# Kernel tuning notes

Measured on AMD Instinct MI355X. Metric: run time of the kernel, lower is better.

## Reference

```python
import jax, jax.numpy as jnp
import numpy as np


def setup_inputs() -> dict:
    key = jax.random.key(0)
    ks = jax.random.split(key, 5)
    B, D, W = 8, 768, 128
    scale = 1.0 / np.sqrt(D)
    return {
        "x": jax.random.normal(ks[0], (B, D, W, W), dtype=jnp.float32),
        "in_proj_w": jax.random.normal(ks[1], (3 * D, D), dtype=jnp.float32) * scale,
        "in_proj_b": jax.random.normal(ks[2], (3 * D,), dtype=jnp.float32) * 0.01,
        "out_w": jax.random.normal(ks[3], (D, D), dtype=jnp.float32) * scale,
        "out_b": jax.random.normal(ks[4], (D,), dtype=jnp.float32) * 0.01,
        "num_heads": 12,
        "num_tokens": 8,
    }


def reference(x, in_proj_w, in_proj_b, out_w, out_b, num_heads, num_tokens):
    B, D, Wd, Hd = x.shape
    nt = num_tokens
    gs = Hd // nt            # grid (block) size
    T = nt * nt              # number of blocks / queries
    S = gs * gs              # k/v tokens per block
    h = num_heads
    hd = D // h

    # ---- query: adaptive avg pool to (nt, nt), flatten, permute -> (B, T, D)
    q = x.reshape(B, D, nt, gs, nt, gs).mean(axis=(3, 5))      # (B, D, nt, nt)
    q = q.reshape(B, D, T).transpose(0, 2, 1)                   # (B, T, D)

    # ---- key/value: faithful reproduction of unfold + view(x.size()) + reshape
    # torch: kv_perm (B,W,H,D) -> unfold -> (B, nt, nt, D, gs, gs) contiguous,
    # then reinterpreted flat as (B, W*H, D) (scrambles channel/pixel layout).
    t = x.transpose(0, 2, 3, 1)                                 # (B, W, H, D)
    t = t.reshape(B, nt, gs, nt, gs, D).transpose(0, 1, 3, 5, 2, 4)  # (B,nt,nt,D,gs,gs)
    kv = t.reshape(B, T, S, D)                                  # chunked into T blocks of S tokens

    # ---- in-projections (torch MultiheadAttention packed weights)
    Wq, Wk, Wv = in_proj_w[:D], in_proj_w[D:2 * D], in_proj_w[2 * D:]
    bq, bk, bv = in_proj_b[:D], in_proj_b[D:2 * D], in_proj_b[2 * D:]
    qp = (q @ Wq.T + bq).reshape(B, T, h, hd)                   # (B, T, h, hd)
    kp = (kv @ Wk.T + bk).reshape(B, T, S, h, hd)               # (B, T, S, h, hd)
    vp = (kv @ Wv.T + bv).reshape(B, T, S, h, hd)

    # ---- block-local single-query attention, batched over all T blocks
    scores = jnp.einsum("bthd,btshd->bths", qp, kp) / np.sqrt(hd)  # (B, T, h, S)
    attn = jax.nn.softmax(scores, axis=-1)
    ctx = jnp.einsum("bths,btshd->bthd", attn, vp).reshape(B, T, D)

    # ---- out projection
    return ctx @ out_w.T + out_b                                # (B, T, D)
```

## Files before the change

kernel.cpp:

```cpp
#include <hip/hip_runtime.h>
#include <hip/hip_bf16.h>

#define D_ 768
#define W_ 128
#define T_ 64
#define S_ 256
#define H_ 12
#define HH_ 6
#define BT_ 512

__device__ __forceinline__ unsigned short f2bf(float f) {
  unsigned u = __float_as_uint(f);
  u = (u + 0x7FFFu + ((u >> 16) & 1u)) >> 16;
  return (unsigned short)u;
}
__device__ __forceinline__ float bfu(unsigned s) {
  return __uint_as_float(s << 16);
}

__global__ __launch_bounds__(384) void k_pack(const float* __restrict__ x,
                                              unsigned short* __restrict__ packed,
                                              float* __restrict__ q) {
  const int blk  = blockIdx.x;
  const int cc   = blk & 15;
  const int tjp  = (blk >> 4) & 3;
  const int ti   = (blk >> 6) & 7;
  const int b    = blk >> 9;
  const int tid  = threadIdx.x;
  const int c8   = tid & 7;
  const int ch   = tid >> 3;
  const int btl  = c8 >> 2;
  const int btg0 = b*64 + ti*8 + tjp*2;
  const int ch0  = cc * 48;

  __shared__ unsigned short tile[48][2][260];
  __shared__ float poolsc[48][2];

  const float* xcol = x + (size_t)b*D_*16384 + (size_t)(ch0 + ch)*16384
                        + (16*ti)*128 + 32*tjp + c8*4;

  float psum = 0.f;
  #pragma unroll
  for (int r = 0; r < 16; ++r) {
    const float4 v = *(const float4*)(xcol + r*128);
    const int px = r*16 + (c8 & 3)*4;
    unsigned lo = (unsigned)f2bf(v.x) | ((unsigned)f2bf(v.y) << 16);
    unsigned hi = (unsigned)f2bf(v.z) | ((unsigned)f2bf(v.w) << 16);
    *(uint2*)&tile[ch][btl][px] = make_uint2(lo, hi);
    psum += (v.x + v.y) + (v.z + v.w);
  }
  psum += __shfl_xor(psum, 1);
  psum += __shfl_xor(psum, 2);
  if ((c8 & 3) == 0) poolsc[ch][btl] = psum;
  __syncthreads();

  for (int ii = tid; ii < 512; ii += 384) {
    const int bl = ii >> 8, p = ii & 255;
    unsigned short* pbt = packed + ((size_t)(btg0 + bl)*16 + cc)*D_*16;
    #pragma unroll
    for (int c = 0; c < 3; ++c) {
      unsigned u[8];
      #pragma unroll
      for (int k2 = 0; k2 < 8; ++k2) {
        const unsigned a  = tile[3*(2*k2)     + c][bl][p];
        const unsigned b2 = tile[3*(2*k2 + 1) + c][bl][p];
        u[k2] = a | (b2 << 16);
      }
      unsigned short* dst = pbt + (size_t)(c*256 + p)*16;
      *(uint4*)(dst)     = make_uint4(u[0], u[1], u[2], u[3]);
      *(uint4*)(dst + 8) = make_uint4(u[4], u[5], u[6], u[7]);
    }
  }
  if (tid < 96) {
    const int ch2 = tid >> 1, bl = tid & 1;
    q[(size_t)(btg0 + bl)*D_ + ch0 + ch2] = poolsc[ch2][bl] * (1.0f/256.0f);
  }
}

__global__ __launch_bounds__(256) void k_qkf(const float* __restrict__ q,
                                             const float* __restrict__ ipw,
                                             const float* __restrict__ ipb,
                                             unsigned short* __restrict__ qkout) {
  const int h   = blockIdx.x >> 5;
  const int btc = blockIdx.x & 31;
  const int bt0 = btc * 16;
  const int tid = threadIdx.x;
  const int i = tid & 63, qw = tid >> 6;
  __shared__ float wt[64][65];
  __shared__ float at[16][65];
  __shared__ float qps[16][72];

  {
    const float* Wr = ipw + (size_t)h*64*D_;
    float acc[4] = {0,0,0,0};
    for (int dc = 0; dc < D_; dc += 64) {
      #pragma unroll
      for (int k = 0; k < 4; ++k) {
        const int idx = k*256 + tid;
        const int r = idx >> 4, c4 = idx & 15;
        *(float4*)&wt[r][c4*4] = *(const float4*)(Wr + (size_t)r*D_ + dc + c4*4);
      }
      {
        const int r = tid >> 4, c4 = tid & 15;
        *(float4*)&at[r][c4*4] = *(const float4*)(q + (size_t)(bt0 + r)*D_ + dc + c4*4);
      }
      __syncthreads();
      #pragma unroll
      for (int dd = 0; dd < 64; ++dd) {
        const float wv = wt[i][dd];
        #pragma unroll
        for (int k = 0; k < 4; ++k)
          acc[k] += at[qw + k*4][dd] * wv;
      }
      __syncthreads();
    }
    const float bqv = ipb[h*64 + i];
    #pragma unroll
    for (int k = 0; k < 4; ++k)
      qps[qw + k*4][i] = acc[k] + bqv;
  }
  __syncthreads();

  for (int ddc = 0; ddc < D_; ddc += 64) {
    #pragma unroll
    for (int k = 0; k < 4; ++k) {
      const int idx = k*256 + tid;
      const int r = idx >> 4, c4 = idx & 15;
      *(float4*)&wt[r][c4*4] = *(const float4*)(ipw + (size_t)(D_ + h*64 + r)*D_ + ddc + c4*4);
    }
    __syncthreads();
    float acc2[4] = {0,0,0,0};
    #pragma unroll 8
    for (int kk = 0; kk < 64; ++kk) {
      const float w = wt[kk][i];
      #pragma unroll
      for (int k = 0; k < 4; ++k)
        acc2[k] += qps[qw + k*4][kk] * w;
    }
    #pragma unroll
    for (int k = 0; k < 4; ++k)
      qkout[((size_t)(bt0 + qw + k*4)*H_ + h)*D_ + ddc + i] = f2bf(acc2[k] * 0.125f);
    __syncthreads();
  }
}

__global__ __launch_bounds__(256) void k_attn3(const unsigned short* __restrict__ packed,
                                               const unsigned short* __restrict__ qkin,
                                               float* __restrict__ wout) {
  const int bt = blockIdx.x >> 1;
  const int hg = blockIdx.x & 1;
  const int tid = threadIdx.x;
  const int wv = tid >> 6, lane = tid & 63;
  __shared__ float pool_lds[HH_ * D_];
  __shared__ float sc[HH_][S_];

  {
    const uint4* src = (const uint4*)(qkin + ((size_t)bt*H_ + hg*HH_)*D_);
    #pragma unroll
    for (int k = 0; k < 3; ++k) {
      const int idx = k*256 + tid;
      if (idx < 576) {
        const uint4 v = src[idx];
        float* d = pool_lds + idx*8;
        d[0] = bfu(v.x & 0xFFFFu); d[1] = bfu(v.x >> 16);
        d[2] = bfu(v.y & 0xFFFFu); d[3] = bfu(v.y >> 16);
        d[4] = bfu(v.z & 0xFFFFu); d[5] = bfu(v.z >> 16);
        d[6] = bfu(v.w & 0xFFFFu); d[7] = bfu(v.w >> 16);
      }
    }
  }
  __syncthreads();

  float acc[HH_][4];
  #pragma unroll
  for (int h = 0; h < HH_; ++h)
    #pragma unroll
    for (int j = 0; j < 4; ++j) acc[h][j] = 0.f;

  {
    const unsigned short* pb = packed + ((size_t)bt*16 + (lane >> 2))*D_*16 + (lane & 3)*4;
    const int d0 = wv * 192;
    short4 pv[4];
    #pragma unroll
    for (int dd = 0; dd < 4; ++dd)
      pv[dd] = *(const short4*)(pb + (size_t)(d0 + dd)*16);
    #pragma unroll 2
    for (int d4 = 0; d4 < 48; ++d4) {
      const int d = d0 + d4*4;
      short4 nx[4];
      if (d4 < 47) {
        #pragma unroll
        for (int dd = 0; dd < 4; ++dd)
          nx[dd] = *(const short4*)(pb + (size_t)(d + 4 + dd)*16);
      }
      float f[4][4];
      #pragma unroll
      for (int dd = 0; dd < 4; ++dd) {
        f[dd][0] = bfu((unsigned)(unsigned short)pv[dd].x);
        f[dd][1] = bfu((unsigned)(unsigned short)pv[dd].y);
        f[dd][2] = bfu((unsigned)(unsigned short)pv[dd].z);
        f[dd][3] = bfu((unsigned)(unsigned short)pv[dd].w);
      }
      #pragma unroll
      for (int h = 0; h < HH_; ++h) {
        const float4 qv = *(const float4*)&pool_lds[h*D_ + d];
        #pragma unroll
        for (int j = 0; j < 4; ++j)
          acc[h][j] += qv.x*f[0][j] + qv.y*f[1][j] + qv.z*f[2][j] + qv.w*f[3][j];
      }
      #pragma unroll
      for (int dd = 0; dd < 4; ++dd) pv[dd] = nx[dd];
    }
  }
  __syncthreads();

  if (wv == 0) {
    #pragma unroll
    for (int h = 0; h < HH_; ++h)
      *(float4*)&sc[h][lane*4] = make_float4(acc[h][0], acc[h][1], acc[h][2], acc[h][3]);
  } else {
    float* dstp = pool_lds + (size_t)(wv - 1)*(HH_*S_);
    #pragma unroll
    for (int h = 0; h < HH_; ++h)
      *(float4*)&dstp[h*S_ + lane*4] = make_float4(acc[h][0], acc[h][1], acc[h][2], acc[h][3]);
  }
  __syncthreads();
  #pragma unroll
  for (int h = 0; h < HH_; ++h)
    sc[h][tid] += pool_lds[0*(HH_*S_) + h*S_ + tid]
                + pool_lds[1*(HH_*S_) + h*S_ + tid]
                + pool_lds[2*(HH_*S_) + h*S_ + tid];
  __syncthreads();

  if (wv < 3) {
    #pragma unroll
    for (int hh = 0; hh < 2; ++hh) {
      const int h = wv*2 + hh;
      float4 v = *(const float4*)(&sc[h][lane*4]);
      float m = fmaxf(fmaxf(v.x, v.y), fmaxf(v.z, v.w));
      #pragma unroll
      for (int off = 32; off > 0; off >>= 1) m = fmaxf(m, __shfl_xor(m, off));
      const float e0 = __expf(v.x - m), e1 = __expf(v.y - m),
                  e2 = __expf(v.z - m), e3 = __expf(v.w - m);
      float ss = (e0+e1)+(e2+e3);
      #pragma unroll
      for (int off = 32; off > 0; off >>= 1) ss += __shfl_xor(ss, off);
      const float inv = 1.0f / ss;
      *(float4*)(&sc[h][lane*4]) = make_float4(e0*inv, e1*inv, e2*inv, e3*inv);
    }
  }
  __syncthreads();

  float wacc[HH_][3];
  #pragma unroll
  for (int h = 0; h < HH_; ++h) { wacc[h][0]=0.f; wacc[h][1]=0.f; wacc[h][2]=0.f; }
  const unsigned short* prow = packed + (size_t)bt*16*D_*16;
  uint4 pv3[3];
  #pragma unroll
  for (int c = 0; c < 3; ++c)
    pv3[c] = *(const uint4*)(prow + ((size_t)0*D_ + c*256 + tid)*16);
  #pragma unroll 2
  for (int s8 = 0; s8 < 32; ++s8) {
    uint4 nx3[3];
    if (s8 < 31) {
      const int t = s8 + 1;
      #pragma unroll
      for (int c = 0; c < 3; ++c)
        nx3[c] = *(const uint4*)(prow + ((size_t)(t >> 1)*D_ + c*256 + tid)*16 + (t & 1)*8);
    }
    float f[3][8];
    #pragma unroll
    for (int c = 0; c < 3; ++c) {
      f[c][0] = bfu(pv3[c].x & 0xFFFFu); f[c][1] = bfu(pv3[c].x >> 16);
      f[c][2] = bfu(pv3[c].y & 0xFFFFu); f[c][3] = bfu(pv3[c].y >> 16);
      f[c][4] = bfu(pv3[c].z & 0xFFFFu); f[c][5] = bfu(pv3[c].z >> 16);
      f[c][6] = bfu(pv3[c].w & 0xFFFFu); f[c][7] = bfu(pv3[c].w >> 16);
    }
    #pragma unroll
    for (int h = 0; h < HH_; ++h) {
      const float4 a0 = *(const float4*)&sc[h][s8*8];
      const float4 a1 = *(const float4*)&sc[h][s8*8 + 4];
      #pragma unroll
      for (int c = 0; c < 3; ++c)
        wacc[h][c] += a0.x*f[c][0] + a0.y*f[c][1] + a0.z*f[c][2] + a0.w*f[c][3]
                    + a1.x*f[c][4] + a1.y*f[c][5] + a1.z*f[c][6] + a1.w*f[c][7];
    }
    #pragma unroll
    for (int c = 0; c < 3; ++c) pv3[c] = nx3[c];
  }
  float* wp = wout + ((size_t)bt*H_ + hg*HH_)*D_;
  #pragma unroll
  for (int h = 0; h < HH_; ++h)
    #pragma unroll
    for (int c = 0; c < 3; ++c)
      wp[h*D_ + c*256 + tid] = wacc[h][c];
}

__global__ __launch_bounds__(256) void k_ctx(const float* __restrict__ wbuf,
                                             const float* __restrict__ ipw,
                                             const float* __restrict__ ipb,
                                             float* __restrict__ ctx) {
  const int h = blockIdx.x >> 6;
  const int bt0 = (blockIdx.x & 63) * 8;
  const int tid = threadIdx.x;
  const float* Wv = ipw + (size_t)2*D_*D_ + (size_t)h*64*D_;
  __shared__ float wt[64][65];
  __shared__ float at[8][65];
  const int i = tid & 63, qw = tid >> 6;
  float acc[2] = {0,0};
  for (int dc = 0; dc < D_; dc += 64) {
    #pragma unroll
    for (int k = 0; k < 4; ++k) {
      const int idx = k*256 + tid;
      const int r = idx >> 4, c4 = idx & 15;
      *(float4*)&wt[r][c4*4] = *(const float4*)(Wv + (size_t)r*D_ + dc + c4*4);
    }
    if (tid < 128) {
      const int r = tid >> 4, c4 = tid & 15;
      *(float4*)&at[r][c4*4] = *(const float4*)(wbuf + ((size_t)(bt0 + r)*H_ + h)*D_ + dc + c4*4);
    }
    __syncthreads();
    #pragma unroll
    for (int dd = 0; dd < 64; ++dd) {
      const float wv = wt[i][dd];
      #pragma unroll
      for (int k = 0; k < 2; ++k)
        acc[k] += at[qw + k*4][dd] * wv;
    }
    __syncthreads();
  }
  const float bvv = ipb[2*D_ + h*64 + i];
  #pragma unroll
  for (int k = 0; k < 2; ++k)
    ctx[(size_t)(bt0 + qw + k*4)*D_ + h*64 + i] = acc[k] + bvv;
}

__global__ __launch_bounds__(256) void k_out(const float* __restrict__ ctx,
                                             const float* __restrict__ ow,
                                             const float* __restrict__ ob,
                                             float* __restrict__ out) {
  const int jt = blockIdx.x >> 6;
  const int bt0 = (blockIdx.x & 63) * 8;
  const int tid = threadIdx.x;
  const float* Wr = ow + (size_t)jt*64*D_;
  __shared__ float wt[64][65];
  __shared__ float at[8][65];
  const int i = tid & 63, qw = tid >> 6;
  float acc[2] = {0,0};
  for (int dc = 0; dc < D_; dc += 64) {
    #pragma unroll
    for (int k = 0; k < 4; ++k) {
      const int idx = k*256 + tid;
      const int r = idx >> 4, c4 = idx & 15;
      *(float4*)&wt[r][c4*4] = *(const float4*)(Wr + (size_t)r*D_ + dc + c4*4);
    }
    if (tid < 128) {
      const int r = tid >> 4, c4 = tid & 15;
      *(float4*)&at[r][c4*4] = *(const float4*)(ctx + (size_t)(bt0 + r)*D_ + dc + c4*4);
    }
    __syncthreads();
    #pragma unroll
    for (int dd = 0; dd < 64; ++dd) {
      const float wv = wt[i][dd];
      #pragma unroll
      for (int k = 0; k < 2; ++k)
        acc[k] += at[qw + k*4][dd] * wv;
    }
    __syncthreads();
  }
  const float obv = ob[jt*64 + i];
  #pragma unroll
  for (int k = 0; k < 2; ++k)
    out[(size_t)(bt0 + qw + k*4)*D_ + jt*64 + i] = acc[k] + obv;
}

__global__ __launch_bounds__(256) void k_q(const float* __restrict__ x, float* __restrict__ q) {
  const int bd = blockIdx.x;
  const int tid = threadIdx.x;
  const float4* xp = (const float4*)(x + (size_t)bd * (W_*W_));
  float acc[8] = {0,0,0,0,0,0,0,0};
  #pragma unroll
  for (int k = 0; k < 16; ++k) {
    float4 v = xp[k*256 + tid];
    acc[k>>1] += (v.x + v.y) + (v.z + v.w);
  }
  __shared__ float part[256][9];
  #pragma unroll
  for (int i = 0; i < 8; ++i) part[tid][i] = acc[i];
  __syncthreads();
  if (tid < 64) {
    const int ti = tid >> 3, tj = tid & 7;
    float s = 0.f;
    #pragma unroll
    for (int m = 0; m < 8; ++m)
      #pragma unroll
      for (int n = 0; n < 4; ++n)
        s += part[m*32 + tj*4 + n][ti];
    const int b = bd / D_, d = bd - b*D_;
    q[(size_t)(b*T_ + tid)*D_ + d] = s * (1.0f/256.0f);
  }
}

__global__ __launch_bounds__(256) void k_attn(const float* __restrict__ x,
                                              const unsigned short* __restrict__ qkin,
                                              float* __restrict__ wout) {
  const int bt = blockIdx.x;
  const int b = bt >> 6, t = bt & 63;
  const int ti = t >> 3, tj = t & 7;
  const int tid = threadIdx.x;
  __shared__ float qkl[H_*D_];
  __shared__ float sc[H_][S_];
  const float* xb = x + (size_t)b*D_*W_*W_ + ti*16*W_ + tj*16;
  {
    const uint4* src = (const uint4*)(qkin + (size_t)bt*H_*D_);
    #pragma unroll
    for (int k = 0; k < 5; ++k) {
      const int idx = k*256 + tid;
      if (idx < 1152) {
        const uint4 v = src[idx];
        float* d = qkl + idx*8;
        d[0] = bfu(v.x & 0xFFFFu); d[1] = bfu(v.x >> 16);
        d[2] = bfu(v.y & 0xFFFFu); d[3] = bfu(v.y >> 16);
        d[4] = bfu(v.z & 0xFFFFu); d[5] = bfu(v.z >> 16);
        d[6] = bfu(v.w & 0xFFFFu); d[7] = bfu(v.w >> 16);
      }
    }
  }
  __syncthreads();
  float acc[H_];
  #pragma unroll
  for (int h = 0; h < H_; ++h) acc[h] = 0.f;
  #pragma unroll
  for (int c = 0; c < 3; ++c) {
    const float* chp = xb + (size_t)(3*tid + c)*(W_*W_);
    for (int blk = 0; blk < 8; ++blk) {
      float4 v[8];
      #pragma unroll
      for (int u = 0; u < 8; ++u) {
        const int pg = blk*8 + u;
        v[u] = *(const float4*)(chp + (pg>>2)*W_ + (pg&3)*4);
      }
      const int dbase = c*256 + blk*32;
      #pragma unroll
      for (int h = 0; h < H_; ++h) {
        const float4* qh = (const float4*)(qkl + h*D_ + dbase);
        float s0 = 0.f;
        #pragma unroll
        for (int u = 0; u < 8; ++u) {
          const float4 qq = qh[u];
          s0 += qq.x*v[u].x + qq.y*v[u].y + qq.z*v[u].z + qq.w*v[u].w;
        }
        acc[h] += s0;
      }
    }
  }
  #pragma unroll
  for (int h = 0; h < H_; ++h) sc[h][tid] = acc[h];
  __syncthreads();
  {
    const int wv = tid >> 6, lane = tid & 63;
    #pragma unroll
    for (int hh = 0; hh < 3; ++hh) {
      const int h = wv*3 + hh;
      float4 v = *(const float4*)(&sc[h][lane*4]);
      float m = fmaxf(fmaxf(v.x, v.y), fmaxf(v.z, v.w));
      #pragma unroll
      for (int off = 32; off > 0; off >>= 1) m = fmaxf(m, __shfl_xor(m, off));
      const float e0 = __expf(v.x - m), e1 = __expf(v.y - m),
                  e2 = __expf(v.z - m), e3 = __expf(v.w - m);
      float ss = (e0+e1)+(e2+e3);
      #pragma unroll
      for (int off = 32; off > 0; off >>= 1) ss += __shfl_xor(ss, off);
      const float inv = 1.0f / ss;
      *(float4*)(&sc[h][lane*4]) = make_float4(e0*inv, e1*inv, e2*inv, e3*inv);
    }
  }
  __syncthreads();
  float wacc[H_][3];
  #pragma unroll
  for (int h = 0; h < H_; ++h) { wacc[h][0]=0.f; wacc[h][1]=0.f; wacc[h][2]=0.f; }
  const float* xp0 = xb + (tid>>4)*W_ + (tid&15);
  for (int s = 0; s < S_; ++s) {
    const float p0 = xp0[(size_t)(3*s+0)*(W_*W_)];
    const float p1 = xp0[(size_t)(3*s+1)*(W_*W_)];
    const float p2 = xp0[(size_t)(3*s+2)*(W_*W_)];
    #pragma unroll
    for (int h = 0; h < H_; ++h) {
      const float at = sc[h][s];
      wacc[h][0] += at*p0; wacc[h][1] += at*p1; wacc[h][2] += at*p2;
    }
  }
  float* wp = wout + (size_t)bt*H_*D_;
  #pragma unroll
  for (int h = 0; h < H_; ++h)
    #pragma unroll
    for (int c = 0; c < 3; ++c)
      wp[h*D_ + c*256 + tid] = wacc[h][c];
}

extern "C" void kernel_launch(void* const* d_in, const int* in_sizes, int n_in,
                              void* d_out, int out_size, void* d_ws, size_t ws_size,
                              hipStream_t stream) {
  const float* x   = (const float*)d_in[0];
  const float* ipw = (const float*)d_in[1];
  const float* ipb = (const float*)d_in[2];
  const float* ow  = (const float*)d_in[3];
  const float* ob  = (const float*)d_in[4];
  float* out = (float*)d_out;

  float* q    = (float*)d_ws;
  float* qp   = q    + (size_t)BT_*D_;
  unsigned short* qk = (unsigned short*)(qp + (size_t)BT_*D_);
  float* wb   = qp   + (size_t)BT_*D_ + (size_t)BT_*H_*D_;
  float* ctxb = wb   + (size_t)BT_*H_*D_;
  unsigned short* packed = (unsigned short*)(ctxb + (size_t)BT_*D_);

  const size_t need_main = ((size_t)BT_*D_*3 + (size_t)BT_*H_*D_*2) * 4
                         + (size_t)BT_*D_*S_*2;

  if (ws_size >= need_main) {
    k_pack <<<dim3(4096), dim3(384), 0, stream>>>(x, packed, q);
    k_qkf  <<<dim3(384),  dim3(256), 0, stream>>>(q, ipw, ipb, qk);
    k_attn3<<<dim3(1024), dim3(256), 0, stream>>>(packed, qk, wb);
    k_ctx  <<<dim3(768),  dim3(256), 0, stream>>>(wb, ipw, ipb, ctxb);
    k_out  <<<dim3(768),  dim3(256), 0, stream>>>(ctxb, ow, ob, out);
  } else {
    k_q    <<<dim3(8*D_), dim3(256), 0, stream>>>(x, q);
    k_qkf  <<<dim3(384),  dim3(256), 0, stream>>>(q, ipw, ipb, qk);
    k_attn <<<dim3(BT_),  dim3(256), 0, stream>>>(x, qk, wb);
    k_ctx  <<<dim3(768),  dim3(256), 0, stream>>>(wb, ipw, ipb, ctxb);
    k_out  <<<dim3(768),  dim3(256), 0, stream>>>(ctxb, ow, ob, out);
  }
}
```

Measured before the change: 422.9 us.

## Split fused q/k-fold kernel into two parallel kernels and store attention output as bf16

The fused k_qkf kernel, which ran on only 384 blocks, is split in two. k_qp computes the query projection over 768 blocks, and k_fold folds it through Wk over 2304 blocks, giving more parallelism and better occupancy. The attention-weighted intermediate buffer wb is now written in bf16 instead of fp32, halving its write and read traffic between k_attn3 and k_ctx. The split costs an extra kernel launch and a qp round-trip through global memory, and bf16 storage adds rounding error to the intermediate.

```diff
diff --git a/kernel.cpp b/kernel.cpp
--- a/kernel.cpp
+++ b/kernel.cpp
@@ -77,76 +77,86 @@
   }
 }
 
-__global__ __launch_bounds__(256) void k_qkf(const float* __restrict__ q,
-                                             const float* __restrict__ ipw,
-                                             const float* __restrict__ ipb,
-                                             unsigned short* __restrict__ qkout) {
-  const int h   = blockIdx.x >> 5;
-  const int btc = blockIdx.x & 31;
-  const int bt0 = btc * 16;
-  const int tid = threadIdx.x;
+__global__ __launch_bounds__(256) void k_qp(const float* __restrict__ q,
+                                            const float* __restrict__ ipw,
+                                            const float* __restrict__ ipb,
+                                            float* __restrict__ qp) {
+  const int jt = blockIdx.x >> 6;
+  const int bt0 = (blockIdx.x & 63) * 8;
+  const int tid = threadIdx.x;
+  const float* Wr = ipw + (size_t)jt*64*D_;
+  __shared__ float wt[64][65];
+  __shared__ float at[8][65];
   const int i = tid & 63, qw = tid >> 6;
-  __shared__ float wt[64][65];
-  __shared__ float at[16][65];
-  __shared__ float qps[16][72];
-
-  {
-    const float* Wr = ipw + (size_t)h*64*D_;
-    float acc[4] = {0,0,0,0};
-    for (int dc = 0; dc < D_; dc += 64) {
-      #pragma unroll
-      for (int k = 0; k < 4; ++k) {
-        const int idx = k*256 + tid;
-        const int r = idx >> 4, c4 = idx & 15;
-        *(float4*)&wt[r][c4*4] = *(const float4*)(Wr + (size_t)r*D_ + dc + c4*4);
-      }
-      {
-        const int r = tid >> 4, c4 = tid & 15;
-        *(float4*)&at[r][c4*4] = *(const float4*)(q + (size_t)(bt0 + r)*D_ + dc + c4*4);
-      }
-      __syncthreads();
-      #pragma unroll
-      for (int dd = 0; dd < 64; ++dd) {
-        const float wv = wt[i][dd];
-        #pragma unroll
-        for (int k = 0; k < 4; ++k)
-          acc[k] += at[qw + k*4][dd] * wv;
-      }
-      __syncthreads();
-    }
-    const float bqv = ipb[h*64 + i];
-    #pragma unroll
-    for (int k = 0; k < 4; ++k)
-      qps[qw + k*4][i] = acc[k] + bqv;
-  }
-  __syncthreads();
-
-  for (int ddc = 0; ddc < D_; ddc += 64) {
+  float acc[2] = {0,0};
+  for (int dc = 0; dc < D_; dc += 64) {
     #pragma unroll
     for (int k = 0; k < 4; ++k) {
       const int idx = k*256 + tid;
       const int r = idx >> 4, c4 = idx & 15;
-      *(float4*)&wt[r][c4*4] = *(const float4*)(ipw + (size_t)(D_ + h*64 + r)*D_ + ddc + c4*4);
+      *(float4*)&wt[r][c4*4] = *(const float4*)(Wr + (size_t)r*D_ + dc + c4*4);
+    }
+    if (tid < 128) {
+      const int r = tid >> 4, c4 = tid & 15;
+      *(float4*)&at[r][c4*4] = *(const float4*)(q + (size_t)(bt0 + r)*D_ + dc + c4*4);
     }
     __syncthreads();
-    float acc2[4] = {0,0,0,0};
-    #pragma unroll 8
-    for (int kk = 0; kk < 64; ++kk) {
-      const float w = wt[kk][i];
-      #pragma unroll
-      for (int k = 0; k < 4; ++k)
-        acc2[k] += qps[qw + k*4][kk] * w;
-    }
-    #pragma unroll
-    for (int k = 0; k < 4; ++k)
-      qkout[((size_t)(bt0 + qw + k*4)*H_ + h)*D_ + ddc + i] = f2bf(acc2[k] * 0.125f);
+    #pragma unroll
+    for (int dd = 0; dd < 64; ++dd) {
+      const float wv = wt[i][dd];
+      #pragma unroll
+      for (int k = 0; k < 2; ++k)
+        acc[k] += at[qw + k*4][dd] * wv;
+    }
     __syncthreads();
   }
+  const float bqv = ipb[jt*64 + i];
+  #pragma unroll
+  for (int k = 0; k < 2; ++k)
+    qp[(size_t)(bt0 + qw + k*4)*D_ + jt*64 + i] = acc[k] + bqv;
+}
+
+__global__ __launch_bounds__(256) void k_fold(const float* __restrict__ qp,
+                                              const float* __restrict__ ipw,
+                                              unsigned short* __restrict__ qkout) {
+  const int btc = blockIdx.x & 15;
+  const int nt  = blockIdx.x >> 4;
+  const int h   = nt / 12;
+  const int ddc = (nt % 12) * 64;
+  const int bt0 = btc * 32;
+  const int tid = threadIdx.x;
+  __shared__ float qpl[32][68];
+  __shared__ float wkl[64][68];
+  #pragma unroll
+  for (int k = 0; k < 2; ++k) {
+    const int idx = k*256 + tid;
+    const int r = idx >> 4, c4 = idx & 15;
+    *(float4*)&qpl[r][c4*4] = *(const float4*)(qp + (size_t)(bt0 + r)*D_ + h*64 + c4*4);
+  }
+  #pragma unroll
+  for (int k = 0; k < 4; ++k) {
+    const int idx = k*256 + tid;
+    const int r = idx >> 4, c4 = idx & 15;
+    *(float4*)&wkl[r][c4*4] = *(const float4*)(ipw + (size_t)(D_ + h*64 + r)*D_ + ddc + c4*4);
+  }
+  __syncthreads();
+  const int i = tid & 63, qw = tid >> 6;
+  float acc[8] = {0,0,0,0,0,0,0,0};
+  #pragma unroll 8
+  for (int kk = 0; kk < 64; ++kk) {
+    const float w = wkl[kk][i];
+    #pragma unroll
+    for (int k = 0; k < 8; ++k)
+      acc[k] += qpl[qw + k*4][kk] * w;
+  }
+  #pragma unroll
+  for (int k = 0; k < 8; ++k)
+    qkout[((size_t)(bt0 + qw + k*4)*H_ + h)*D_ + ddc + i] = f2bf(acc[k] * 0.125f);
 }
 
 __global__ __launch_bounds__(256) void k_attn3(const unsigned short* __restrict__ packed,
                                                const unsigned short* __restrict__ qkin,
-                                               float* __restrict__ wout) {
+                                               unsigned short* __restrict__ wout) {
   const int bt = blockIdx.x >> 1;
   const int hg = blockIdx.x & 1;
   const int tid = threadIdx.x;
@@ -288,15 +298,15 @@
     #pragma unroll
     for (int c = 0; c < 3; ++c) pv3[c] = nx3[c];
   }
-  float* wp = wout + ((size_t)bt*H_ + hg*HH_)*D_;
+  unsigned short* wp = wout + ((size_t)bt*H_ + hg*HH_)*D_;
   #pragma unroll
   for (int h = 0; h < HH_; ++h)
     #pragma unroll
     for (int c = 0; c < 3; ++c)
-      wp[h*D_ + c*256 + tid] = wacc[h][c];
-}
-
-__global__ __launch_bounds__(256) void k_ctx(const float* __restrict__ wbuf,
+      wp[h*D_ + c*256 + tid] = f2bf(wacc[h][c]);
+}
+
+__global__ __launch_bounds__(256) void k_ctx(const unsigned short* __restrict__ wbuf,
                                              const float* __restrict__ ipw,
                                              const float* __restrict__ ipb,
                                              float* __restrict__ ctx) {
@@ -317,7 +327,11 @@
     }
     if (tid < 128) {
       const int r = tid >> 4, c4 = tid & 15;
-      *(float4*)&at[r][c4*4] = *(const float4*)(wbuf + ((size_t)(bt0 + r)*H_ + h)*D_ + dc + c4*4);
+      const uint2 v = *(const uint2*)(wbuf + ((size_t)(bt0 + r)*H_ + h)*D_ + dc + c4*4);
+      at[r][c4*4 + 0] = bfu(v.x & 0xFFFFu);
+      at[r][c4*4 + 1] = bfu(v.x >> 16);
+      at[r][c4*4 + 2] = bfu(v.y & 0xFFFFu);
+      at[r][c4*4 + 3] = bfu(v.y >> 16);
     }
     __syncthreads();
     #pragma unroll
@@ -403,7 +417,7 @@
 
 __global__ __launch_bounds__(256) void k_attn(const float* __restrict__ x,
                                               const unsigned short* __restrict__ qkin,
-                                              float* __restrict__ wout) {
+                                              unsigned short* __restrict__ wout) {
   const int bt = blockIdx.x;
   const int b = bt >> 6, t = bt & 63;
   const int ti = t >> 3, tj = t & 7;
@@ -490,12 +504,12 @@
       wacc[h][0] += at*p0; wacc[h][1] += at*p1; wacc[h][2] += at*p2;
     }
   }
-  float* wp = wout + (size_t)bt*H_*D_;
+  unsigned short* wp = wout + (size_t)bt*H_*D_;
   #pragma unroll
   for (int h = 0; h < H_; ++h)
     #pragma unroll
     for (int c = 0; c < 3; ++c)
-      wp[h*D_ + c*256 + tid] = wacc[h][c];
+      wp[h*D_ + c*256 + tid] = f2bf(wacc[h][c]);
 }
 
 extern "C" void kernel_launch(void* const* d_in, const int* in_sizes, int n_in,
@@ -511,8 +525,8 @@
   float* q    = (float*)d_ws;
   float* qp   = q    + (size_t)BT_*D_;
   unsigned short* qk = (unsigned short*)(qp + (size_t)BT_*D_);
-  float* wb   = qp   + (size_t)BT_*D_ + (size_t)BT_*H_*D_;
-  float* ctxb = wb   + (size_t)BT_*H_*D_;
+  unsigned short* wb = (unsigned short*)(qp + (size_t)BT_*D_ + (size_t)BT_*H_*D_);
+  float* ctxb = qp + (size_t)BT_*D_ + (size_t)BT_*H_*D_*2;
   unsigned short* packed = (unsigned short*)(ctxb + (size_t)BT_*D_);
 
   const size_t need_main = ((size_t)BT_*D_*3 + (size_t)BT_*H_*D_*2) * 4
@@ -520,13 +534,15 @@
 
   if (ws_size >= need_main) {
     k_pack <<<dim3(4096), dim3(384), 0, stream>>>(x, packed, q);
-    k_qkf  <<<dim3(384),  dim3(256), 0, stream>>>(q, ipw, ipb, qk);
+    k_qp   <<<dim3(768),  dim3(256), 0, stream>>>(q, ipw, ipb, qp);
+    k_fold <<<dim3(2304), dim3(256), 0, stream>>>(qp, ipw, qk);
     k_attn3<<<dim3(1024), dim3(256), 0, stream>>>(packed, qk, wb);
     k_ctx  <<<dim3(768),  dim3(256), 0, stream>>>(wb, ipw, ipb, ctxb);
     k_out  <<<dim3(768),  dim3(256), 0, stream>>>(ctxb, ow, ob, out);
   } else {
     k_q    <<<dim3(8*D_), dim3(256), 0, stream>>>(x, q);
-    k_qkf  <<<dim3(384),  dim3(256), 0, stream>>>(q, ipw, ipb, qk);
+    k_qp   <<<dim3(768),  dim3(256), 0, stream>>>(q, ipw, ipb, qp);
+    k_fold <<<dim3(2304), dim3(256), 0, stream>>>(qp, ipw, qk);
     k_attn <<<dim3(BT_),  dim3(256), 0, stream>>>(x, qk, wb);
     k_ctx  <<<dim3(768),  dim3(256), 0, stream>>>(wb, ipw, ipb, ctxb);
     k_out  <<<dim3(768),  dim3(256), 0, stream>>>(ctxb, ow, ob, out);
```

After: 383.3 us. 1.1x faster.
